# Kernel optimization log

Hardware: AMD Instinct MI355X
Metric: run time of the kernel (lower is better)

Reference implementation:

```python
import jax, jax.numpy as jnp
import numpy as np

KS = 16
FREQ = jnp.array([0., 1., 2., 4., 8., 16., 32., 64.], dtype=jnp.float32)  # [0]+[2^i], d=8
TWO_PI = 2.0 * np.pi


def softplus_b10(x):
    # torch F.softplus(x, beta=10, threshold=1): linear when beta*x > threshold
    bx = 10.0 * x
    return jnp.where(bx > 1.0, x, jnp.log1p(jnp.exp(jnp.minimum(bx, 1.0))) / 10.0)


def grid_sample_2d(img, gx, gy):
    # img: (C, H, W) complex; gx,gy: (N,) in [-1,1]. Bilinear, align_corners=True,
    # zero padding -- matches torch.nn.functional.grid_sample. Returns (C, N).
    C, H, W = img.shape
    ix = (gx + 1.0) * 0.5 * (W - 1)
    iy = (gy + 1.0) * 0.5 * (H - 1)
    ix0 = jnp.floor(ix)
    iy0 = jnp.floor(iy)
    wx = ix - ix0
    wy = iy - iy0

    def corner(iyc, ixc, w):
        valid = (ixc >= 0) & (ixc <= W - 1) & (iyc >= 0) & (iyc <= H - 1)
        ii = jnp.clip(ixc, 0, W - 1).astype(jnp.int32)
        jj = jnp.clip(iyc, 0, H - 1).astype(jnp.int32)
        return img[:, jj, ii] * (w * valid)[None, :]

    return (corner(iy0, ix0, (1 - wx) * (1 - wy))
            + corner(iy0, ix0 + 1, wx * (1 - wy))
            + corner(iy0 + 1, ix0, (1 - wx) * wy)
            + corner(iy0 + 1, ix0 + 1, wx * wy))


def batch_irfft(P, x):
    # P: (ks, d, N) complex; x: (N,) in [-1,1]. Trig-weighted inverse rFFT reduce.
    xx = (x + 1.0) * 0.5
    ang = TWO_PI * xx[:, None] * FREQ[None, :]            # (N, d)
    scale = jnp.where(FREQ > 0, 2.0, 1.0)
    c = jnp.cos(ang) * scale
    s = jnp.sin(ang) * scale
    return jnp.einsum('kdn,nd->kn', P.real, c) - jnp.einsum('kdn,nd->kn', P.imag, s)


def reference(xyz, bound, alpha_params, Pu_re, Pu_im, Pv_re, Pv_im, Pw_re, Pw_im):
    alpha = softplus_b10(alpha_params)[0]
    Pu = jnp.fft.ifftn((Pu_re + 1j * Pu_im) * alpha, axes=(3, 4))  # (1,ks,dx,Ny,Nz)
    Pv = jnp.fft.ifftn((Pv_re + 1j * Pv_im) * alpha, axes=(2, 4))  # (1,ks,Nx,dy,Nz)
    Pw = jnp.fft.ifftn((Pw_re + 1j * Pw_im) * alpha, axes=(2, 3))  # (1,ks,Nx,Ny,dz)

    xyzn = xyz / bound
    xs, ys, zs = xyzn[:, 0], xyzn[:, 1], xyzn[:, 2]
    N = xs.shape[0]

    ks, dx = Pu.shape[1], Pu.shape[2]
    dy = Pv.shape[3]
    dz = Pw.shape[4]

    # Pu: sample over (Ny, Nz) plane; grid (x=zs -> width Nz, y=ys -> height Ny)
    Px = grid_sample_2d(Pu[0].reshape(ks * dx, Pu.shape[3], Pu.shape[4]), zs, ys).reshape(ks, dx, N)
    # Pv: transpose (ks,Nx,dy,Nz)->(ks,dy,Nx,Nz); grid (x=zs -> Nz, y=xs -> Nx)
    Py = grid_sample_2d(jnp.swapaxes(Pv[0], 1, 2).reshape(ks * dy, Pv.shape[2], Pv.shape[4]), zs, xs).reshape(ks, dy, N)
    # Pw: transpose (ks,Nx,Ny,dz)->(ks,dz,Ny,Nx); grid (x=xs -> Nx, y=ys -> Ny)
    Pz = grid_sample_2d(jnp.swapaxes(Pw[0], 1, 3).reshape(ks * dz, Pw.shape[3], Pw.shape[2]), xs, ys).reshape(ks, dz, N)

    P = batch_irfft(Px, xs) + batch_irfft(Py, ys) + batch_irfft(Pz, zs)  # (ks, N)
    return P.T  # (N, ks)


def setup_inputs() -> dict:
    key = jax.random.key(0)
    ks = jax.random.split(key, 8)
    N = 131072
    xyz = jax.random.uniform(ks[0], (N, 3), dtype=jnp.float32, minval=-1.0, maxval=1.0)
    scale = 0.05
    return {
        'xyz': xyz,
        'bound': 1.0,
        'alpha_params': jnp.full((1,), 0.001, dtype=jnp.float32),
        'Pu_re': scale * jax.random.normal(ks[1], (1, KS, 8, 160, 160), dtype=jnp.float32),
        'Pu_im': scale * jax.random.normal(ks[2], (1, KS, 8, 160, 160), dtype=jnp.float32),
        'Pv_re': scale * jax.random.normal(ks[3], (1, KS, 160, 8, 160), dtype=jnp.float32),
        'Pv_im': scale * jax.random.normal(ks[4], (1, KS, 160, 8, 160), dtype=jnp.float32),
        'Pw_re': scale * jax.random.normal(ks[5], (1, KS, 160, 160, 8), dtype=jnp.float32),
        'Pw_im': scale * jax.random.normal(ks[6], (1, KS, 160, 160, 8), dtype=jnp.float32),
    }
```

## Files before the change

### kernel.cpp

```cpp
#include <hip/hip_runtime.h>
#include <hip/hip_bf16.h>

#define G 160
#define GM1 159
#define KD 128
#define KP 320
#define PLANE_U 3276800
#define NBUCK 4096
#define TWO_PI_F 6.28318530717958647692f

#define TSCALE 256.0f
#define TSCALE_INV 0.00390625f

typedef __attribute__((ext_vector_type(8))) short bf16x8;
typedef __attribute__((ext_vector_type(4))) float f32x4;
typedef _Float16 half2t __attribute__((ext_vector_type(2)));
typedef __fp16 fp16x2 __attribute__((ext_vector_type(2)));

__device__ __forceinline__ unsigned short f2bf(float x) {
    unsigned u = __float_as_uint(x);
    unsigned r = (u + 0x7FFFu + ((u >> 16) & 1u)) >> 16;
    return (unsigned short)r;
}
__device__ __forceinline__ unsigned int packbf(float re, float im) {
    union { __hip_bfloat162 h; unsigned int u; } cv;
    cv.h = __float22bfloat162_rn(make_float2(re, im));
    return cv.u;
}
__device__ __forceinline__ half2t cvtpk(float a, float b) {
    union { fp16x2 f; half2t h; } cv;
    cv.f = __builtin_amdgcn_cvt_pkrtz(a, b);
    return cv.h;
}
__device__ __forceinline__ unsigned int packh(float re, float im) {
    union { fp16x2 f; unsigned int u; } cv;
    cv.f = __builtin_amdgcn_cvt_pkrtz(re, im);
    return cv.u;
}
__device__ __forceinline__ half2t u2h2(unsigned int u) {
    union { unsigned int u; half2t h; } cv;
    cv.u = u;
    return cv.h;
}
__device__ __forceinline__ float fdot2h(half2t a, half2t b, float acc) {
#if __has_builtin(__builtin_amdgcn_fdot2)
    return __builtin_amdgcn_fdot2(a, b, acc, false);
#else
    return acc + (float)a.x * (float)b.x + (float)a.y * (float)b.y;
#endif
}
__device__ __forceinline__ unsigned int wim_of(unsigned int u) {
    return ((u << 16) | (u >> 16)) ^ 0x00008000u;
}
__device__ __forceinline__ unsigned part1by2(unsigned x) {
    x &= 0x3FF;
    x = (x | (x << 16)) & 0xFF0000FFu;
    x = (x | (x << 8))  & 0x0300F00Fu;
    x = (x | (x << 4))  & 0x030C30C3u;
    x = (x | (x << 2))  & 0x09249249u;
    return x;
}
__device__ __forceinline__ unsigned morton_key(float x, float y, float z) {
    int cx = min(max((int)((x + 1.0f) * 8.0f), 0), 15);
    int cy = min(max((int)((y + 1.0f) * 8.0f), 0), 15);
    int cz = min(max((int)((z + 1.0f) * 8.0f), 0), 15);
    return part1by2(cx) | (part1by2(cy) << 1) | (part1by2(cz) << 2);
}

__global__ __launch_bounds__(256) void k_prep(
    const float* __restrict__ Pw_re, const float* __restrict__ Pw_im,
    unsigned int* __restrict__ Apw, unsigned short* __restrict__ Wre,
    unsigned int* __restrict__ counts)
{
    __shared__ unsigned int sT[64 * 33];
    int b = blockIdx.x;
    int tid = threadIdx.x;
    if (b < 16) {
        counts[b * 256 + tid] = 0;
        return;
    }
    if (b < 216) {
        int idx = (b - 16) * 256 + tid;
        int r = idx / KP, kp = idx - r * KP;
        int q = kp >> 1;
        int m = (r * q) % G;
        float th = (float)m * (TWO_PI_F / (float)G);
        float s, c;
        __sincosf(th, &s, &c);
        Wre[idx] = f2bf(((kp & 1) == 0 ? c : -s) * (1.0f / (float)G));
        return;
    }
    int b2 = b - 216;
    int k  = b2 / 100;
    int rem = b2 - k * 100;
    int pc = rem / 5;
    int q0 = (rem - pc * 5) * 32;

    int i = tid & 63, qo = tid >> 6;
    size_t base = (size_t)k * 204800 + (size_t)pc * 64 + i;
    #pragma unroll
    for (int qc = 0; qc < 8; qc++) {
        int q = q0 + qo * 8 + qc;
        float r  = Pw_re[base + (size_t)q * 1280];
        float im = Pw_im[base + (size_t)q * 1280];
        sT[i * 33 + qo * 8 + qc] = packbf(r, im);
    }
    __syncthreads();
    int qp = tid & 31, mo = tid >> 5;
    #pragma unroll
    for (int mc = 0; mc < 8; mc++) {
        int m = (k * 8 + mo) * G + pc * 8 + mc;
        Apw[(size_t)m * G + q0 + qp] = sT[(mc * 8 + mo) * 33 + qp];
    }
}

__global__ __launch_bounds__(256) void k_hist(
    const float* __restrict__ xyz, const float* __restrict__ bound,
    unsigned int* __restrict__ counts, int N)
{
    int i = blockIdx.x * blockDim.x + threadIdx.x;
    if (i >= N) return;
    float invb = 1.0f / bound[0];
    float x = xyz[3 * i + 0] * invb;
    float y = xyz[3 * i + 1] * invb;
    float z = xyz[3 * i + 2] * invb;
    atomicAdd(&counts[morton_key(x, y, z)], 1u);
}

__global__ __launch_bounds__(1024) void k_scan(
    const unsigned int* __restrict__ counts,
    unsigned int* __restrict__ cursors)
{
    __shared__ unsigned int ws[16];
    int t = threadIdx.x;
    int lane = t & 63, wid = t >> 6;
    unsigned int local[4];
    unsigned int s = 0;
    #pragma unroll
    for (int i = 0; i < 4; i++) { local[i] = counts[t * 4 + i]; s += local[i]; }
    unsigned int sl = s;
    #pragma unroll
    for (int off = 1; off < 64; off <<= 1) {
        unsigned int v = __shfl_up(s, off, 64);
        if (lane >= off) s += v;
    }
    if (lane == 63) ws[wid] = s;
    __syncthreads();
    if (t < 16) {
        unsigned int x = ws[t];
        #pragma unroll
        for (int off = 1; off < 16; off <<= 1) {
            unsigned int v = __shfl_up(x, off, 64);
            if (t >= off) x += v;
        }
        ws[t] = x;
    }
    __syncthreads();
    unsigned int run = s - sl + (wid > 0 ? ws[wid - 1] : 0u);
    #pragma unroll
    for (int i = 0; i < 4; i++) { cursors[t * 4 + i] = run; run += local[i]; }
}

__global__ __launch_bounds__(256) void k_scatter(
    const float* __restrict__ xyz, const float* __restrict__ bound,
    unsigned int* __restrict__ cursors, float4* __restrict__ sxyz, int N)
{
    int i = blockIdx.x * blockDim.x + threadIdx.x;
    if (i >= N) return;
    float invb = 1.0f / bound[0];
    float x = xyz[3 * i + 0] * invb;
    float y = xyz[3 * i + 1] * invb;
    float z = xyz[3 * i + 2] * invb;
    unsigned int pos = atomicAdd(&cursors[morton_key(x, y, z)], 1u);
    sxyz[pos] = make_float4(x, y, z, __int_as_float(i));
}

__global__ __launch_bounds__(512, 4) void k_stage1(
    const float* __restrict__ Pu_re, const float* __restrict__ Pu_im,
    const float* __restrict__ Pv_re, const float* __restrict__ Pv_im,
    const unsigned int* __restrict__ Apw,
    const float* __restrict__ alpha_params,
    const unsigned short* __restrict__ Wre,
    unsigned int* __restrict__ Bfrag)
{
    int tid = threadIdx.x;
    int w = tid >> 6, lane = tid & 63;
    int col = lane & 15, g4 = lane >> 4;
    int gw = blockIdx.x * 8 + w;
    int plane = gw / 1280;
    int mtl = gw - plane * 1280;

    float ap = alpha_params[0];
    float bxv = 10.0f * ap;
    float alpha = (bxv > 1.0f) ? ap : log1pf(expf(fminf(bxv, 1.0f))) * 0.1f;
    alpha *= TSCALE;

    bf16x8 afr[10];
    if (plane == 2) {
        const unsigned int* a2 = Apw + (size_t)(mtl * 16 + col) * G + g4 * 4;
        #pragma unroll
        for (int t = 0; t < 10; t++) {
            union { uint4 u; bf16x8 b; } cv;
            cv.u = *(const uint4*)(a2 + t * 16);
            afr[t] = cv.b;
        }
    } else {
        const float *Ar, *Ai; int sd_, sp_;
        if (plane == 0) { Ar = Pu_re; Ai = Pu_im; sd_ = 25600; sp_ = 160; }
        else            { Ar = Pv_re; Ai = Pv_im; sd_ = 160;   sp_ = 1280; }
        int m = mtl * 16 + col;
        int k = m / 1280; int rm = m - k * 1280;
        int d = rm / 160; int p = rm - d * 160;
        size_t abase = (size_t)k * 204800 + (size_t)d * sd_ + (size_t)p * sp_ + g4 * 4;
        #pragma unroll
        for (int t = 0; t < 10; t++) {
            float4 vr = *(const float4*)(Ar + abase + t * 16);
            float4 vi = *(const float4*)(Ai + abase + t * 16);
            union { unsigned int u[4]; bf16x8 b; } cv;
            cv.u[0] = packbf(vr.x, vi.x); cv.u[1] = packbf(vr.y, vi.y);
            cv.u[2] = packbf(vr.z, vi.z); cv.u[3] = packbf(vr.w, vi.w);
            afr[t] = cv.b;
        }
    }

    unsigned int* Bpl = Bfrag + (size_t)plane * PLANE_U;
    int kd = mtl / 10, pt = mtl - kd * 10;

    for (int lt2 = 0; lt2 < 5; lt2++) {
        int ltA = lt2 * 2, ltB = lt2 * 2 + 1;
        f32x4 arA = (f32x4)(0.f), aiA = (f32x4)(0.f);
        f32x4 arB = (f32x4)(0.f), aiB = (f32x4)(0.f);
        const unsigned short* wpA = &Wre[(ltA * 16 + col) * KP + g4 * 8];
        const unsigned short* wpB = &Wre[(ltB * 16 + col) * KP + g4 * 8];
        #pragma unroll
        for (int t = 0; t < 10; t++) {
            union { uint4 u; bf16x8 b; } crA, ciA, crB, ciB;
            crA.u = *(const uint4*)(wpA + t * 32);
            crB.u = *(const uint4*)(wpB + t * 32);
            ciA.u.x = wim_of(crA.u.x); ciA.u.y = wim_of(crA.u.y);
            ciA.u.z = wim_of(crA.u.z); ciA.u.w = wim_of(crA.u.w);
            ciB.u.x = wim_of(crB.u.x); ciB.u.y = wim_of(crB.u.y);
            ciB.u.z = wim_of(crB.u.z); ciB.u.w = wim_of(crB.u.w);
            arA = __builtin_amdgcn_mfma_f32_16x16x32_bf16(afr[t], crA.b, arA, 0, 0, 0);
            aiA = __builtin_amdgcn_mfma_f32_16x16x32_bf16(afr[t], ciA.b, aiA, 0, 0, 0);
            arB = __builtin_amdgcn_mfma_f32_16x16x32_bf16(afr[t], crB.b, arB, 0, 0, 0);
            aiB = __builtin_amdgcn_mfma_f32_16x16x32_bf16(afr[t], ciB.b, aiB, 0, 0, 0);
        }
        uint4 o;
        o.x = packbf(alpha * arA[0], alpha * aiA[0]);
        o.y = packbf(alpha * arA[1], alpha * aiA[1]);
        o.z = packbf(alpha * arA[2], alpha * aiA[2]);
        o.w = packbf(alpha * arA[3], alpha * aiA[3]);
        *(uint4*)(Bpl + (size_t)(kd * 10 + ltA) * 2560 + pt * 256 + lane * 4) = o;
        o.x = packbf(alpha * arB[0], alpha * aiB[0]);
        o.y = packbf(alpha * arB[1], alpha * aiB[1]);
        o.z = packbf(alpha * arB[2], alpha * aiB[2]);
        o.w = packbf(alpha * arB[3], alpha * aiB[3]);
        *(uint4*)(Bpl + (size_t)(kd * 10 + ltB) * 2560 + pt * 256 + lane * 4) = o;
    }
}

__global__ __launch_bounds__(640) void k_stage2(
    const unsigned int* __restrict__ Bfrag,
    const unsigned short* __restrict__ Wre,
    unsigned int* __restrict__ Tall)
{
    __shared__ __align__(16) unsigned int sB[20480];
    int tid = threadIdx.x;
    int w = tid >> 6, lane = tid & 63;
    int col = lane & 15, g4 = lane >> 4;
    int kdo = blockIdx.x;
    int lt  = blockIdx.y;
    int plane = blockIdx.z;

    const unsigned int* Bp = Bfrag + (size_t)plane * PLANE_U;
    #pragma unroll
    for (int i = 0; i < 8; i++) {
        uint4 v = *(const uint4*)(Bp + ((size_t)(kdo * 8 + i) * 10 + lt) * 2560 + tid * 4);
        *(uint4*)(sB + i * 2560 + tid * 4) = v;
    }

    bf16x8 wfr[10];
    const unsigned short* wp = &Wre[(w * 16 + col) * KP + g4 * 8];
    #pragma unroll
    for (int t = 0; t < 10; t++)
        wfr[t] = *(const bf16x8*)(wp + t * 32);

    __syncthreads();

    f32x4 ar[8], ai[8];
    #pragma unroll
    for (int i = 0; i < 8; i++) { ar[i] = (f32x4)(0.f); ai[i] = (f32x4)(0.f); }

    #pragma unroll
    for (int t = 0; t < 10; t++) {
        union { bf16x8 b; uint4 u; } cr, ci;
        cr.b = wfr[t];
        ci.u.x = wim_of(cr.u.x); ci.u.y = wim_of(cr.u.y);
        ci.u.z = wim_of(cr.u.z); ci.u.w = wim_of(cr.u.w);
        #pragma unroll
        for (int kq = 0; kq < 8; kq++) {
            bf16x8 bf = *(const bf16x8*)&sB[kq * 2560 + (t * 64 + lane) * 4];
            ar[kq] = __builtin_amdgcn_mfma_f32_16x16x32_bf16(cr.b, bf, ar[kq], 0, 0, 0);
            ai[kq] = __builtin_amdgcn_mfma_f32_16x16x32_bf16(ci.b, bf, ai[kq], 0, 0, 0);
        }
    }

    unsigned int* Tp = Tall + (size_t)plane * PLANE_U;
    #pragma unroll
    for (int reg = 0; reg < 4; reg++) {
        int j = w * 16 + g4 * 4 + reg;
        int l = lt * 16 + col;
        uint4 o0, o1;
        o0.x = packh(ar[0][reg], ai[0][reg]);
        o0.y = packh(ar[1][reg], ai[1][reg]);
        o0.z = packh(ar[2][reg], ai[2][reg]);
        o0.w = packh(ar[3][reg], ai[3][reg]);
        o1.x = packh(ar[4][reg], ai[4][reg]);
        o1.y = packh(ar[5][reg], ai[5][reg]);
        o1.z = packh(ar[6][reg], ai[6][reg]);
        o1.w = packh(ar[7][reg], ai[7][reg]);
        size_t ta = ((size_t)(j * G + l)) * KD + kdo * 8;
        *(uint4*)(Tp + ta)     = o0;
        *(uint4*)(Tp + ta + 4) = o1;
    }
}

__device__ __forceinline__ void plane_addr(const unsigned int* __restrict__ T,
    float gy, float gx, int k, const unsigned int** cp, float* wv)
{
    float iy = (gy + 1.0f) * (0.5f * (float)GM1);
    float ix = (gx + 1.0f) * (0.5f * (float)GM1);
    float iy0f = floorf(iy), ix0f = floorf(ix);
    float wy = iy - iy0f, wx = ix - ix0f;
    int iy0 = (int)iy0f, ix0 = (int)ix0f;
    int iy1 = min(iy0 + 1, GM1), ix1 = min(ix0 + 1, GM1);
    iy0 = max(min(iy0, GM1), 0); ix0 = max(min(ix0, GM1), 0);
    iy1 = max(iy1, 0); ix1 = max(ix1, 0);
    cp[0] = &T[(size_t)(iy0 * G + ix0) * KD + k * 8];
    cp[1] = &T[(size_t)(iy0 * G + ix1) * KD + k * 8];
    cp[2] = &T[(size_t)(iy1 * G + ix0) * KD + k * 8];
    cp[3] = &T[(size_t)(iy1 * G + ix1) * KD + k * 8];
    wv[0] = (1.f - wx) * (1.f - wy);
    wv[1] = wx * (1.f - wy);
    wv[2] = (1.f - wx) * wy;
    wv[3] = wx * wy;
}

__device__ __forceinline__ float plane_math(const uint4* va, const uint4* vb,
                                            const float* wv, float fc)
{
    float s1v, c1v;
    __sincosf(TWO_PI_F * fc, &s1v, &c1v);
    half2t tw[8];
    tw[0] = u2h2(0x00003C00u);
    float cd = c1v, sd = s1v;
    tw[1] = cvtpk(cd + cd, -(sd + sd));
    #pragma unroll
    for (int d = 2; d < 8; d++) {
        float t2 = cd + cd;
        float cn = __builtin_fmaf(t2, cd, -1.0f);
        float sn = t2 * sd;
        cd = cn; sd = sn;
        tw[d] = cvtpk(cd + cd, -(sd + sd));
    }
    const unsigned int* a0 = (const unsigned int*)&va[0];
    const unsigned int* a1 = (const unsigned int*)&va[1];
    const unsigned int* a2 = (const unsigned int*)&va[2];
    const unsigned int* a3 = (const unsigned int*)&va[3];
    const unsigned int* b0 = (const unsigned int*)&vb[0];
    const unsigned int* b1 = (const unsigned int*)&vb[1];
    const unsigned int* b2 = (const unsigned int*)&vb[2];
    const unsigned int* b3 = (const unsigned int*)&vb[3];
    float d0 = 0.f, d1 = 0.f, d2 = 0.f, d3 = 0.f;
    #pragma unroll
    for (int d = 0; d < 4; d++) {
        half2t t = tw[d];
        d0 = fdot2h(u2h2(a0[d]), t, d0);
        d1 = fdot2h(u2h2(a1[d]), t, d1);
        d2 = fdot2h(u2h2(a2[d]), t, d2);
        d3 = fdot2h(u2h2(a3[d]), t, d3);
    }
    #pragma unroll
    for (int d = 0; d < 4; d++) {
        half2t t = tw[d + 4];
        d0 = fdot2h(u2h2(b0[d]), t, d0);
        d1 = fdot2h(u2h2(b1[d]), t, d1);
        d2 = fdot2h(u2h2(b2[d]), t, d2);
        d3 = fdot2h(u2h2(b3[d]), t, d3);
    }
    float acc = wv[0] * d0;
    acc = __builtin_fmaf(wv[1], d1, acc);
    acc = __builtin_fmaf(wv[2], d2, acc);
    acc = __builtin_fmaf(wv[3], d3, acc);
    return acc;
}

__global__ __launch_bounds__(256, 3) void k_sample(
    const float4* __restrict__ sxyz,
    const unsigned int* __restrict__ Tu, const unsigned int* __restrict__ Tv,
    const unsigned int* __restrict__ Tw,
    float* __restrict__ out, int N)
{
    int tid = threadIdx.x;
    int k = tid & 15;
    int nblocks = (N + 15) / 16;
    int seg = blockIdx.x & 7;
    int segblocks = nblocks >> 3;
    int pid = (seg * segblocks + (blockIdx.x >> 3)) * 16 + (tid >> 4);
    if (pid >= N) return;

    float4 pw = sxyz[pid];
    int n = __float_as_int(pw.w);
    float x = pw.x, y = pw.y, z = pw.z;

    const unsigned int* cp[3][4];
    float wv[3][4];
    plane_addr(Tu, y, z, k, cp[0], wv[0]);
    plane_addr(Tv, x, z, k, cp[1], wv[1]);
    plane_addr(Tw, y, x, k, cp[2], wv[2]);

    uint4 va[3][4], vb[3][4];
    #pragma unroll
    for (int pl = 0; pl < 3; pl++)
        #pragma unroll
        for (int c = 0; c < 4; c++) {
            va[pl][c] = *(const uint4*)cp[pl][c];
            vb[pl][c] = *(const uint4*)(cp[pl][c] + 4);
        }

    float acc = plane_math(va[0], vb[0], wv[0], (x + 1.0f) * 0.5f)
              + plane_math(va[1], vb[1], wv[1], (y + 1.0f) * 0.5f)
              + plane_math(va[2], vb[2], wv[2], (z + 1.0f) * 0.5f);
    out[n * 16 + k] = acc * TSCALE_INV;
}

extern "C" void kernel_launch(void* const* d_in, const int* in_sizes, int n_in,
                              void* d_out, int out_size, void* d_ws, size_t ws_size,
                              hipStream_t stream) {
    const float* xyz          = (const float*)d_in[0];
    const float* bound        = (const float*)d_in[1];
    const float* alpha_params = (const float*)d_in[2];
    const float* Pu_re = (const float*)d_in[3];
    const float* Pu_im = (const float*)d_in[4];
    const float* Pv_re = (const float*)d_in[5];
    const float* Pv_im = (const float*)d_in[6];
    const float* Pw_re = (const float*)d_in[7];
    const float* Pw_im = (const float*)d_in[8];
    float* out = (float*)d_out;
    int N = in_sizes[0] / 3;

    char* ws = (char*)d_ws;
    unsigned short* Wre  = (unsigned short*)(ws);
    unsigned int*   Apw  = (unsigned int*)(ws + 102400);
    unsigned int*   Bfr  = (unsigned int*)(ws + 102400 + 13107200);
    unsigned int*   Tall = (unsigned int*)(ws + 102400 + 13107200 + 39321600);
    char*           ws2  = ws + 102400 + 13107200 + 39321600 + 39321600;
    unsigned int*   counts  = (unsigned int*)(ws2);
    unsigned int*   cursors = (unsigned int*)(ws2 + 16384);
    float4*         sxyz    = (float4*)(ws2 + 32768);
    unsigned int*   Tu   = Tall;
    unsigned int*   Tv   = Tall + (size_t)PLANE_U;
    unsigned int*   Tw   = Tall + (size_t)2 * PLANE_U;

    k_prep<<<1816, 256, 0, stream>>>(Pw_re, Pw_im, Apw, Wre, counts);
    k_hist<<<(N + 255) / 256, 256, 0, stream>>>(xyz, bound, counts, N);
    k_scan<<<1, 1024, 0, stream>>>(counts, cursors);
    k_scatter<<<(N + 255) / 256, 256, 0, stream>>>(xyz, bound, cursors, sxyz, N);
    k_stage1<<<480, 512, 0, stream>>>(Pu_re, Pu_im, Pv_re, Pv_im, Apw,
                                      alpha_params, Wre, Bfr);
    k_stage2<<<dim3(16, 10, 3), 640, 0, stream>>>(Bfr, Wre, Tall);
    k_sample<<<(N + 15) / 16, 256, 0, stream>>>(sxyz, Tu, Tv, Tw, out, N);
}
```

Measured before the change: 282.4 us.

## Stage DFT twiddle fragments in LDS and derive upper rows by conjugate symmetry

Stage1 now copies the first six 16-row tiles of the bf16 DFT weight matrix into shared memory, pre-swizzled into MFMA fragment order. Each wave then reads its B fragments from LDS instead of global memory. The last four row tiles are not loaded; they are rebuilt from the stored rows using the conjugate symmetry of the DFT matrix (row 160-r), with sign-bit flips and halfword swaps. This trades about 60KB of LDS per block and a block-wide barrier for fewer global or L2 weight reads, which may lower occupancy given launch_bounds(512,4).

```diff
diff --git a/kernel.cpp b/kernel.cpp
--- a/kernel.cpp
+++ b/kernel.cpp
@@ -51,6 +51,9 @@
 }
 __device__ __forceinline__ unsigned int wim_of(unsigned int u) {
     return ((u << 16) | (u >> 16)) ^ 0x00008000u;
+}
+__device__ __forceinline__ unsigned int rot16(unsigned int u) {
+    return (u << 16) | (u >> 16);
 }
 __device__ __forceinline__ unsigned part1by2(unsigned x) {
     x &= 0x3FF;
@@ -183,12 +186,23 @@
     const unsigned short* __restrict__ Wre,
     unsigned int* __restrict__ Bfrag)
 {
+    __shared__ __align__(16) unsigned short sW[30720];
     int tid = threadIdx.x;
     int w = tid >> 6, lane = tid & 63;
     int col = lane & 15, g4 = lane >> 4;
     int gw = blockIdx.x * 8 + w;
     int plane = gw / 1280;
     int mtl = gw - plane * 1280;
+
+    for (int chunk = tid; chunk < 3840; chunk += 512) {
+        int lt = chunk / 640;
+        int r  = chunk - lt * 640;
+        int t  = r >> 6;
+        int ln = r & 63;
+        int c  = ln & 15, g = ln >> 4;
+        uint4 v = *(const uint4*)&Wre[(lt * 16 + c) * KP + t * 32 + g * 8];
+        *(uint4*)&sW[chunk * 8] = v;
+    }
 
     float ap = alpha_params[0];
     float bxv = 10.0f * ap;
@@ -223,24 +237,68 @@
         }
     }
 
+    __syncthreads();
+
     unsigned int* Bpl = Bfrag + (size_t)plane * PLANE_U;
     int kd = mtl / 10, pt = mtl - kd * 10;
 
-    for (int lt2 = 0; lt2 < 5; lt2++) {
+    #pragma unroll
+    for (int lt2 = 0; lt2 < 3; lt2++) {
         int ltA = lt2 * 2, ltB = lt2 * 2 + 1;
         f32x4 arA = (f32x4)(0.f), aiA = (f32x4)(0.f);
         f32x4 arB = (f32x4)(0.f), aiB = (f32x4)(0.f);
-        const unsigned short* wpA = &Wre[(ltA * 16 + col) * KP + g4 * 8];
-        const unsigned short* wpB = &Wre[(ltB * 16 + col) * KP + g4 * 8];
+        const unsigned short* wpA = &sW[(ltA * 640 + lane) * 8];
+        const unsigned short* wpB = &sW[(ltB * 640 + lane) * 8];
         #pragma unroll
         for (int t = 0; t < 10; t++) {
             union { uint4 u; bf16x8 b; } crA, ciA, crB, ciB;
-            crA.u = *(const uint4*)(wpA + t * 32);
-            crB.u = *(const uint4*)(wpB + t * 32);
+            crA.u = *(const uint4*)(wpA + t * 512);
+            crB.u = *(const uint4*)(wpB + t * 512);
             ciA.u.x = wim_of(crA.u.x); ciA.u.y = wim_of(crA.u.y);
             ciA.u.z = wim_of(crA.u.z); ciA.u.w = wim_of(crA.u.w);
             ciB.u.x = wim_of(crB.u.x); ciB.u.y = wim_of(crB.u.y);
             ciB.u.z = wim_of(crB.u.z); ciB.u.w = wim_of(crB.u.w);
+            arA = __builtin_amdgcn_mfma_f32_16x16x32_bf16(afr[t], crA.b, arA, 0, 0, 0);
+            aiA = __builtin_amdgcn_mfma_f32_16x16x32_bf16(afr[t], ciA.b, aiA, 0, 0, 0);
+            arB = __builtin_amdgcn_mfma_f32_16x16x32_bf16(afr[t], crB.b, arB, 0, 0, 0);
+            aiB = __builtin_amdgcn_mfma_f32_16x16x32_bf16(afr[t], ciB.b, aiB, 0, 0, 0);
+        }
+        uint4 o;
+        o.x = packbf(alpha * arA[0], alpha * aiA[0]);
+        o.y = packbf(alpha * arA[1], alpha * aiA[1]);
+        o.z = packbf(alpha * arA[2], alpha * aiA[2]);
+        o.w = packbf(alpha * arA[3], alpha * aiA[3]);
+        *(uint4*)(Bpl + (size_t)(kd * 10 + ltA) * 2560 + pt * 256 + lane * 4) = o;
+        o.x = packbf(alpha * arB[0], alpha * aiB[0]);
+        o.y = packbf(alpha * arB[1], alpha * aiB[1]);
+        o.z = packbf(alpha * arB[2], alpha * aiB[2]);
+        o.w = packbf(alpha * arB[3], alpha * aiB[3]);
+        *(uint4*)(Bpl + (size_t)(kd * 10 + ltB) * 2560 + pt * 256 + lane * 4) = o;
+    }
+
+    #pragma unroll
+    for (int lt2 = 3; lt2 < 5; lt2++) {
+        int ltA = lt2 * 2, ltB = lt2 * 2 + 1;
+        f32x4 arA = (f32x4)(0.f), aiA = (f32x4)(0.f);
+        f32x4 arB = (f32x4)(0.f), aiB = (f32x4)(0.f);
+        int stA = (col == 0) ? (10 - ltA) : (9 - ltA);
+        int stB = (col == 0) ? (10 - ltB) : (9 - ltB);
+        int sc  = (col == 0) ? 0 : (16 - col);
+        const unsigned short* wpA = &sW[(stA * 640 + g4 * 16 + sc) * 8];
+        const unsigned short* wpB = &sW[(stB * 640 + g4 * 16 + sc) * 8];
+        #pragma unroll
+        for (int t = 0; t < 10; t++) {
+            union { uint4 u; bf16x8 b; } crA, ciA, crB, ciB;
+            uint4 uA = *(const uint4*)(wpA + t * 512);
+            uint4 uB = *(const uint4*)(wpB + t * 512);
+            crA.u.x = uA.x ^ 0x80000000u; crA.u.y = uA.y ^ 0x80000000u;
+            crA.u.z = uA.z ^ 0x80000000u; crA.u.w = uA.w ^ 0x80000000u;
+            ciA.u.x = rot16(uA.x); ciA.u.y = rot16(uA.y);
+            ciA.u.z = rot16(uA.z); ciA.u.w = rot16(uA.w);
+            crB.u.x = uB.x ^ 0x80000000u; crB.u.y = uB.y ^ 0x80000000u;
+            crB.u.z = uB.z ^ 0x80000000u; crB.u.w = uB.w ^ 0x80000000u;
+            ciB.u.x = rot16(uB.x); ciB.u.y = rot16(uB.y);
+            ciB.u.z = rot16(uB.z); ciB.u.w = rot16(uB.w);
             arA = __builtin_amdgcn_mfma_f32_16x16x32_bf16(afr[t], crA.b, arA, 0, 0, 0);
             aiA = __builtin_amdgcn_mfma_f32_16x16x32_bf16(afr[t], ciA.b, aiA, 0, 0, 0);
             arB = __builtin_amdgcn_mfma_f32_16x16x32_bf16(afr[t], crB.b, arB, 0, 0, 0);
```

Measured after the change: 254.7 us. 9.8% less time.
